# Performance work log

Measured on AMD Instinct MI355X. Metric: run time of the kernel, lower is better.

Reference implementation:

```python
import jax, jax.numpy as jnp
import numpy as np

H, B, T = 4, 16, 4000
E, D, A, C, K, O = 512, 512, 128, 10, 101, 512


def setup_inputs() -> dict:
    key = jax.random.key(0)
    ks = jax.random.split(key, 12)
    return {
        "enc_pad": jax.random.normal(ks[0], (B, T, E), jnp.float32),
        "enc_len": jax.random.randint(ks[1], (B,), T // 2, T + 1, jnp.int32),
        "dec_z": jax.random.normal(ks[2], (B, D), jnp.float32),
        "att_prev": jax.random.uniform(ks[3], (H, B, T), jnp.float32) / T,
        # learned parameters (per-head stacks)
        "Wenc": jax.random.normal(ks[4], (H, E, A), jnp.float32) / np.sqrt(E).astype(np.float32),
        "benc": jnp.zeros((H, A), jnp.float32),
        "Wdec": jax.random.normal(ks[5], (H, D, A), jnp.float32) / np.sqrt(D).astype(np.float32),
        "Watt": jax.random.normal(ks[6], (H, C, A), jnp.float32) / np.sqrt(C).astype(np.float32),
        "conv_w": jax.random.normal(ks[7], (H, C, K), jnp.float32) / np.sqrt(K).astype(np.float32),
        "gv": jax.random.normal(ks[8], (H, A), jnp.float32) / np.sqrt(A).astype(np.float32),
        "Wo": jax.random.normal(ks[9], (H * E, O), jnp.float32) / np.sqrt(H * E).astype(np.float32),
        "bo": jnp.zeros((O,), jnp.float32),
    }


def reference(enc_pad, enc_len, dec_z, att_prev, Wenc, benc, Wdec, Watt, conv_w, gv, Wo, bo):
    scaling = 1.0
    Hh, Bb, Tt = att_prev.shape
    Cc, Kk = conv_w.shape[1], conv_w.shape[2]
    pad_l = Kk // 2
    pad_r = Kk // 2 if Kk % 2 == 1 else Kk // 2 - 1
    # location conv: grouped 1D conv over heads. lhs [B,H,Tp], rhs [H*C,1,K]
    x = jnp.pad(att_prev.transpose(1, 0, 2), ((0, 0), (0, 0), (pad_l, pad_r)))
    rhs = conv_w.reshape(Hh * Cc, 1, Kk)
    conv = jax.lax.conv_general_dilated(
        x, rhs, window_strides=(1,), padding='VALID',
        dimension_numbers=('NCH', 'OIH', 'NCH'), feature_group_count=Hh)  # [B,H*C,T]
    conv = conv.reshape(Bb, Hh, Cc, Tt)
    att_conv = jnp.einsum('bhct,hca->bhta', conv, Watt)                    # mlp_att
    enc_proj = jnp.einsum('bte,hea->bhta', enc_pad, Wenc) + benc[None, :, None, :]  # mlp_enc
    dec_proj = jnp.einsum('bd,hda->bha', dec_z, Wdec)[:, :, None, :]       # mlp_dec
    e = jnp.einsum('bhta,ha->bht', jnp.tanh(enc_proj + dec_proj + att_conv), gv)  # gvec
    w = jax.nn.softmax(scaling * e, axis=-1)                               # [B,H,T]
    c = jnp.einsum('bht,bte->bhe', w, enc_pad).reshape(Bb, Hh * enc_pad.shape[-1])
    out = c @ Wo + bo                                                      # mlp_o
    return out, w.transpose(1, 0, 2)  # ws stacked as [H,B,T]
```

## Files before the change

kernel.cpp:

```cpp
#include <hip/hip_runtime.h>
#include <hip/hip_bf16.h>

#define H_ 4
#define B_ 16
#define T_ 4000
#define E_ 512
#define D_ 512
#define A_ 128
#define C_ 10
#define K_ 101
#define O_ 512
#define TC_ 50
#define CH_ (T_ / TC_)

typedef __attribute__((ext_vector_type(4))) float f32x4;
typedef __attribute__((ext_vector_type(8)))  short short8;

#define MFMA16(a, b, c) __builtin_amdgcn_mfma_f32_16x16x32_bf16(a, b, c, 0, 0, 0)

#define GLL16(gp, lp) __builtin_amdgcn_global_load_lds( \
    (const __attribute__((address_space(1))) unsigned int*)(gp), \
    (__attribute__((address_space(3))) unsigned int*)(lp), 16, 0, 0)

static __device__ __forceinline__ unsigned short f2bf(float x) {
  unsigned u = __float_as_uint(x);
  unsigned r = (u + 0x7FFFu + ((u >> 16) & 1u)) >> 16;
  return (unsigned short)r;
}
static __device__ __forceinline__ unsigned pk2(float a, float b) {
  return (unsigned)f2bf(a) | ((unsigned)f2bf(b) << 16);
}
static __device__ __forceinline__ unsigned cvtpk(float lo, float hi) {
  unsigned r;
  asm("v_cvt_pk_bf16_f32 %0, %1, %2" : "=v"(r) : "v"(lo), "v"(hi));
  return r;
}
static __device__ __forceinline__ uint4 packbf8(float4 f0, float4 f1) {
  uint4 u;
  u.x = cvtpk(f0.x, f0.y); u.y = cvtpk(f0.z, f0.w);
  u.z = cvtpk(f1.x, f1.y); u.w = cvtpk(f1.z, f1.w);
  return u;
}
static __device__ __forceinline__ float tanh_fast(float x) {
  return 1.0f - 2.0f / (__expf(2.0f * x) + 1.0f);
}
static __device__ __forceinline__ float bfup(unsigned short u) {
  return __uint_as_float((unsigned)u << 16);
}
static __device__ __forceinline__ int swz(int r) {
  return (r & 3) ^ ((r >> 2) & 3);
}

__global__ __launch_bounds__(256) void k_prepconv(
    const float* __restrict__ Wenc, const float* __restrict__ Watt,
    const float* __restrict__ dec_z, const float* __restrict__ Wdec,
    const float* __restrict__ benc, const float* __restrict__ att_prev,
    const float* __restrict__ conv_w,
    char* __restrict__ wbs2, char* __restrict__ wattb2,
    float* __restrict__ addv4, char* __restrict__ convpad) {
  __shared__ float ap[256 + K_ - 1 + 3];
  __shared__ float cw[C_ * K_];
  const int bid = blockIdx.x;
  const int tid = threadIdx.x;
  if (bid >= 257) {
    const int cid = bid - 257;
    const int bh = cid & 63;
    const int b = bh / H_, h = bh % H_;
    const int t0 = (cid >> 6) * 256;
    const float* src = att_prev + ((size_t)h * B_ + b) * T_;
    for (int i = tid; i < 256 + K_ - 1; i += 256) {
      int tt = t0 - (K_ / 2) + i;
      ap[i] = (tt >= 0 && tt < T_) ? src[tt] : 0.f;
    }
    for (int i = tid; i < C_ * K_; i += 256) cw[i] = conv_w[(size_t)h * C_ * K_ + i];
    __syncthreads();
    const int t = t0 + tid;
    if (t < T_) {
      float s[C_];
#pragma unroll
      for (int c = 0; c < C_; ++c) s[c] = 0.f;
      for (int k = 0; k < K_; ++k) {
        float apv = ap[tid + k];
#pragma unroll
        for (int c = 0; c < C_; ++c) s[c] += cw[c * K_ + k] * apv;
      }
      uint4 u0, u1;
      u0.x = pk2(s[0], s[1]); u0.y = pk2(s[2], s[3]);
      u0.z = pk2(s[4], s[5]); u0.w = pk2(s[6], s[7]);
      u1.x = pk2(s[8], s[9]); u1.y = 0u; u1.z = 0u; u1.w = 0u;
      char* dst = convpad + (size_t)(b * T_ + t) * 128 + h * 32;
      *(uint4*)dst = u0;
      *(uint4*)(dst + 16) = u1;
    }
  } else if (bid < 128) {
    const int c = bid * 256 + tid;
    const int kt = c >> 11;
    const int ci = c & 2047;
    const int col = ci >> 2, cc = ci & 3;
    const int h = col >> 7, a = col & 127;
    const int kk = kt * 32 + ((cc ^ swz(col)) & 3) * 8;
    const float* w = Wenc + ((size_t)h * E_ + kk) * A_ + a;
    uint4 u;
    u.x = pk2(w[0], w[A_]);
    u.y = pk2(w[2 * A_], w[3 * A_]);
    u.z = pk2(w[4 * A_], w[5 * A_]);
    u.w = pk2(w[6 * A_], w[7 * A_]);
    ((uint4*)wbs2)[c] = u;
  } else if (bid == 128) {
#pragma unroll
    for (int q = 0; q < 4; ++q) {
      const int cw2 = q * 256 + tid;
      const int h = cw2 >> 8;
      const int rr = cw2 & 255;
      const int col = rr >> 1, half = rr & 1;
      unsigned short v[8];
#pragma unroll
      for (int j = 0; j < 8; ++j) {
        const int k = half * 8 + j;
        v[j] = (k < C_) ? f2bf(Watt[((size_t)h * C_ + k) * A_ + col]) : (unsigned short)0;
      }
      uint4 u;
      u.x = (unsigned)v[0] | ((unsigned)v[1] << 16);
      u.y = (unsigned)v[2] | ((unsigned)v[3] << 16);
      u.z = (unsigned)v[4] | ((unsigned)v[5] << 16);
      u.w = (unsigned)v[6] | ((unsigned)v[7] << 16);
      ((uint4*)wattb2)[cw2] = u;
    }
  } else {
    const int idx = bid - 129;
    const int b = idx >> 3, h = (idx >> 1) & 3, ks = idx & 1;
    const int a = tid & 127, kh = tid >> 7;
    const int p = ks * 2 + kh;
    const int d0 = p * 128;
    const float* z = dec_z + (size_t)b * D_ + d0;
    const float* w = Wdec + ((size_t)h * D_ + d0) * A_ + a;
    float s = (p == 0) ? benc[h * A_ + a] : 0.f;
#pragma unroll 8
    for (int d = 0; d < 128; ++d) s += z[d] * w[(size_t)d * A_];
    addv4[(((size_t)p * B_ + b) * H_ + h) * A_ + a] = s;
  }
}

__global__ __launch_bounds__(512, 4) void k_fused_e_mfma(
    const float* __restrict__ enc,
    const char*  __restrict__ wbs2,
    const char*  __restrict__ convpad,
    const char*  __restrict__ wattb2,
    const float* __restrict__ addv4,
    const float* __restrict__ gv,
    char* __restrict__ encbf,
    float* __restrict__ e_out) {
  __shared__ char smem[73728];
  const int tid = threadIdx.x;
  const int wv = tid >> 6;
  const int lane = tid & 63, l15 = lane & 15, lg = lane >> 4;
  const int m0 = blockIdx.x * 64;
  const int h = wv >> 1;
  const bool aRole = (wv < 4);

  f32x4 acc[4][4];
#pragma unroll
  for (int i = 0; i < 4; ++i)
#pragma unroll
    for (int j = 0; j < 4; ++j) acc[i][j] = (f32x4){0.f, 0.f, 0.f, 0.f};

  int aOff[4], bOff[4];
#pragma unroll
  for (int q = 0; q < 4; ++q) {
    const int row = q * 16 + l15;
    aOff[q] = row * 64 + (((lg ^ swz(row)) & 3) << 4);
    const int col = wv * 64 + q * 16 + l15;
    bOff[q] = col * 64 + (((lg ^ swz(col)) & 3) << 4);
  }

  const int arow = tid >> 2, ac = tid & 3;
  const int ks = ((ac ^ swz(arow)) & 3) * 8;
  const float* eR = enc + (size_t)(m0 + arow) * E_ + ks;
  const int wOff = arow * 64 + ac * 16;
  char* ebW = encbf + (size_t)(m0 + arow) * 1024 + ks * 2;
  const char* bsrc = wbs2 + (size_t)(wv - 4) * 8192 + lane * 16;
  char* bdstBase = smem + 8192 + (wv - 4) * 8192;

  float4 X0, X1;
  const float* eP = eR + 64;
  const char* bsP = bsrc + 32768;

  if (aRole) {
    float4 c0 = *(const float4*)eR;
    float4 c1 = *(const float4*)(eR + 4);
    X0 = *(const float4*)(eR + 32);
    X1 = *(const float4*)(eR + 36);
    uint4 pkv = packbf8(c0, c1);
    *(uint4*)(smem + wOff) = pkv;
    *(uint4*)ebW = pkv;
    asm volatile("s_waitcnt lgkmcnt(0)" ::: "memory");
  } else {
#pragma unroll
    for (int i = 0; i < 8; ++i)
      GLL16(bsrc + i * 1024, bdstBase + i * 1024);
    asm volatile("s_waitcnt vmcnt(0) lgkmcnt(0)" ::: "memory");
  }
  __builtin_amdgcn_sched_barrier(0);
  __builtin_amdgcn_s_barrier();

#pragma unroll 1
  for (int kt = 0; kt < 16; ++kt) {
    const int cur = kt & 1;
    const char* bufA = smem + cur * 4096;
    const char* bufB = smem + 8192 + cur * 32768;

    if (!aRole && kt < 15) {
      char* d = smem + 8192 + (cur ^ 1) * 32768 + (wv - 4) * 8192;
#pragma unroll
      for (int i = 0; i < 8; ++i)
        GLL16(bsP + i * 1024, d + i * 1024);
    }
    __builtin_amdgcn_sched_barrier(0);

    short8 aF[4];
#pragma unroll
    for (int q = 0; q < 4; ++q) aF[q] = *(const short8*)(bufA + aOff[q]);
#pragma unroll
    for (int qn = 0; qn < 4; ++qn) {
      short8 bF = *(const short8*)(bufB + bOff[qn]);
#pragma unroll
      for (int qm = 0; qm < 4; ++qm)
        acc[qm][qn] = MFMA16(aF[qm], bF, acc[qm][qn]);
    }

    if (aRole) {
      if (kt < 15) {
        uint4 pkv = packbf8(X0, X1);
        *(uint4*)(smem + (cur ^ 1) * 4096 + wOff) = pkv;
        *(uint4*)(ebW + (kt + 1) * 64) = pkv;
      }
      if (kt < 14) {
        X0 = *(const float4*)eP;
        X1 = *(const float4*)(eP + 4);
        eP += 32;
      }
    } else {
      bsP += 32768;
    }

    if (kt < 14) {
      if (aRole)
        asm volatile("s_waitcnt lgkmcnt(0)" ::: "memory");
      else
        asm volatile("s_waitcnt vmcnt(0) lgkmcnt(0)" ::: "memory");
    } else {
      asm volatile("s_waitcnt vmcnt(0) lgkmcnt(0)" ::: "memory");
    }
    __builtin_amdgcn_sched_barrier(0);
    __builtin_amdgcn_s_barrier();
  }

  {
    short8 zf;
#pragma unroll
    for (int i = 0; i < 8; ++i) zf[i] = 0;
    short8 cf[4], wf[4];
#pragma unroll
    for (int q = 0; q < 4; ++q) { cf[q] = zf; wf[q] = zf; }
    if (lg < 2) {
#pragma unroll
      for (int q = 0; q < 4; ++q) {
        const int row = m0 + q * 16 + l15;
        cf[q] = *(const short8*)(convpad + (size_t)row * 128 + h * 32 + lg * 16);
        const int col = (wv & 1) * 64 + q * 16 + l15;
        wf[q] = *(const short8*)(wattb2 + ((size_t)h * 128 + col) * 32 + lg * 16);
      }
    }
#pragma unroll
    for (int qm = 0; qm < 4; ++qm)
#pragma unroll
      for (int qn = 0; qn < 4; ++qn)
        acc[qm][qn] = MFMA16(cf[qm], wf[qn], acc[qm][qn]);
  }

  {
    const unsigned b0w = (unsigned)m0 / 4000u;
    const unsigned b1w = (unsigned)(m0 + 63) / 4000u;
    float av0[4], av1[4], gvr[4];
#pragma unroll
    for (int qn = 0; qn < 4; ++qn) {
      const int col = (wv & 1) * 64 + qn * 16 + l15;
      const int i0 = (int)b0w * 512 + h * 128 + col;
      const int i1 = (int)b1w * 512 + h * 128 + col;
      av0[qn] = addv4[i0] + addv4[8192 + i0] + addv4[16384 + i0] + addv4[24576 + i0];
      av1[qn] = addv4[i1] + addv4[8192 + i1] + addv4[16384 + i1] + addv4[24576 + i1];
      gvr[qn] = gv[h * 128 + col];
    }
    float* Pb = (float*)smem;
#pragma unroll
    for (int qm = 0; qm < 4; ++qm) {
#pragma unroll
      for (int r = 0; r < 4; ++r) {
        const int rowLocal = qm * 16 + lg * 4 + r;
        const unsigned brow = (unsigned)(m0 + rowLocal);
        const unsigned bb = brow / 4000u;
        const int sel = (bb != b0w);
        float s = 0.f;
#pragma unroll
        for (int qn = 0; qn < 4; ++qn)
          s += gvr[qn] * tanh_fast(acc[qm][qn][r] + (sel ? av1[qn] : av0[qn]));
        s += __shfl_xor(s, 1);
        s += __shfl_xor(s, 2);
        s += __shfl_xor(s, 4);
        s += __shfl_xor(s, 8);
        if (l15 == 0) Pb[wv * 64 + rowLocal] = s;
      }
    }
  }
  __syncthreads();
  if (tid < 256) {
    const float* Pb = (const float*)smem;
    const int hh = tid >> 6, r = tid & 63;
    const float ev = Pb[(hh * 2) * 64 + r] + Pb[(hh * 2 + 1) * 64 + r];
    const unsigned brow = (unsigned)(m0 + r);
    const unsigned bb = brow / 4000u;
    const unsigned tt = brow - bb * 4000u;
    e_out[((size_t)bb * H_ + hh) * T_ + tt] = ev;
  }
}

__global__ __launch_bounds__(256) void k_msum(const float* __restrict__ e_in,
                                              float2* __restrict__ msum) {
  const int bh = blockIdx.x;
  const float* er = e_in + (size_t)bh * T_;
  __shared__ float red[256];
  const int tid = threadIdx.x;
  float m = -1e30f;
  for (int t = tid; t < T_; t += 256) m = fmaxf(m, er[t]);
  red[tid] = m;
  __syncthreads();
  for (int s = 128; s > 0; s >>= 1) {
    if (tid < s) red[tid] = fmaxf(red[tid], red[tid + s]);
    __syncthreads();
  }
  m = red[0];
  __syncthreads();
  float sum = 0.f;
  for (int t = tid; t < T_; t += 256) sum += __expf(er[t] - m);
  red[tid] = sum;
  __syncthreads();
  for (int s = 128; s > 0; s >>= 1) {
    if (tid < s) red[tid] += red[tid + s];
    __syncthreads();
  }
  if (tid == 0) msum[bh] = make_float2(m, 1.0f / red[0]);
}

__global__ __launch_bounds__(512) void k_ctx(const char* __restrict__ encbf,
                                             const float* __restrict__ e_in,
                                             const float2* __restrict__ msum,
                                             float* __restrict__ wout,
                                             float* __restrict__ partial) {
  const int b = blockIdx.x, tc = blockIdx.y;
  const int t0 = tc * CH_;
  const int tid = threadIdx.x;
  const int grp = tid >> 7, lt = tid & 127;
  __shared__ float wls[H_ * CH_];
  __shared__ float4 red[3][4][128];
  for (int i = tid; i < H_ * CH_; i += 512) {
    const int h = i / CH_, tt = i - h * CH_;
    const float2 ms = msum[b * H_ + h];
    const float w = __expf(e_in[((size_t)b * H_ + h) * T_ + t0 + tt] - ms.x) * ms.y;
    wls[i] = w;
    wout[((size_t)h * B_ + b) * T_ + t0 + tt] = w;
  }
  __syncthreads();
  float4 a0 = {0,0,0,0}, a1 = {0,0,0,0}, a2 = {0,0,0,0}, a3 = {0,0,0,0};
  const unsigned short* eb = (const unsigned short*)encbf;
  const int tg = grp * 20;
  const size_t ebase = ((size_t)b * T_ + t0 + tg) * 512 + lt * 4;
#pragma unroll 5
  for (int tt = 0; tt < 20; ++tt) {
    const ushort4 v = *(const ushort4*)(eb + ebase + (size_t)tt * 512);
    const float4 x = {bfup(v.x), bfup(v.y), bfup(v.z), bfup(v.w)};
    const float w0 = wls[tg + tt];
    const float w1 = wls[CH_ + tg + tt];
    const float w2 = wls[2 * CH_ + tg + tt];
    const float w3 = wls[3 * CH_ + tg + tt];
    a0.x += w0 * x.x; a0.y += w0 * x.y; a0.z += w0 * x.z; a0.w += w0 * x.w;
    a1.x += w1 * x.x; a1.y += w1 * x.y; a1.z += w1 * x.z; a1.w += w1 * x.w;
    a2.x += w2 * x.x; a2.y += w2 * x.y; a2.z += w2 * x.z; a2.w += w2 * x.w;
    a3.x += w3 * x.x; a3.y += w3 * x.y; a3.z += w3 * x.z; a3.w += w3 * x.w;
  }
  if (grp > 0) {
    red[grp - 1][0][lt] = a0;
    red[grp - 1][1][lt] = a1;
    red[grp - 1][2][lt] = a2;
    red[grp - 1][3][lt] = a3;
  }
  __syncthreads();
  if (grp == 0) {
#pragma unroll
    for (int g = 0; g < 3; ++g) {
      const float4 r0 = red[g][0][lt], r1 = red[g][1][lt];
      const float4 r2 = red[g][2][lt], r3 = red[g][3][lt];
      a0.x += r0.x; a0.y += r0.y; a0.z += r0.z; a0.w += r0.w;
      a1.x += r1.x; a1.y += r1.y; a1.z += r1.z; a1.w += r1.w;
      a2.x += r2.x; a2.y += r2.y; a2.z += r2.z; a2.w += r2.w;
      a3.x += r3.x; a3.y += r3.y; a3.z += r3.z; a3.w += r3.w;
    }
    float4* p4 = (float4*)partial;
    const size_t pbase = (((size_t)tc * B_ + b) * H_) * 128 + lt;
    p4[pbase] = a0;
    p4[pbase + 128] = a1;
    p4[pbase + 256] = a2;
    p4[pbase + 384] = a3;
  }
}

__global__ __launch_bounds__(256) void k_out_part(const float* __restrict__ partial,
                                                  const float* __restrict__ Wo,
                                                  float* __restrict__ p2) {
  const int b = blockIdx.x;
  const int o = blockIdx.y * 256 + threadIdx.x;
  const int kc = blockIdx.z;
  __shared__ float cS[256];
  const int he0 = kc * 256;
  {
    float s = 0.f;
#pragma unroll
    for (int tc = 0; tc < TC_; ++tc)
      s += partial[((size_t)tc * B_ + b) * (H_ * E_) + he0 + threadIdx.x];
    cS[threadIdx.x] = s;
  }
  __syncthreads();
  float s = 0.f;
#pragma unroll 8
  for (int i = 0; i < 256; ++i) s += cS[i] * Wo[(size_t)(he0 + i) * O_ + o];
  p2[((size_t)kc * B_ + b) * O_ + o] = s;
}

__global__ __launch_bounds__(512) void k_out_fin(const float* __restrict__ p2,
                                                 const float* __restrict__ bo,
                                                 float* __restrict__ out) {
  const int b = blockIdx.x, o = threadIdx.x;
  float s = bo[o];
#pragma unroll
  for (int kc = 0; kc < 8; ++kc) s += p2[((size_t)kc * B_ + b) * O_ + o];
  out[b * O_ + o] = s;
}

extern "C" void kernel_launch(void* const* d_in, const int* in_sizes, int n_in,
                              void* d_out, int out_size, void* d_ws, size_t ws_size,
                              hipStream_t stream) {
  (void)in_sizes; (void)n_in; (void)out_size; (void)ws_size;
  const float* enc      = (const float*)d_in[0];
  const float* dec_z    = (const float*)d_in[2];
  const float* att_prev = (const float*)d_in[3];
  const float* Wenc     = (const float*)d_in[4];
  const float* benc     = (const float*)d_in[5];
  const float* Wdec     = (const float*)d_in[6];
  const float* Watt     = (const float*)d_in[7];
  const float* conv_w   = (const float*)d_in[8];
  const float* gv       = (const float*)d_in[9];
  const float* Wo       = (const float*)d_in[10];
  const float* bo       = (const float*)d_in[11];

  float* out  = (float*)d_out;
  float* wout = out + B_ * O_;

  char* wsb = (char*)d_ws;
  float*  e_buf   = (float*)(wsb);
  char*   convpad = wsb + 1024000;
  char*   wbs2    = wsb + 9216000;
  char*   wattb2  = wsb + 9740288;
  float*  addv4   = (float*)(wsb + 9756672);
  float2* msum    = (float2*)(wsb + 9887744);
  float*  partial = (float*)(wsb + 9888256);
  float*  p2      = (float*)(wsb + 16441856);
  char*   encbf   = wsb + 16704000;

  hipLaunchKernelGGL(k_prepconv, dim3(1281), dim3(256), 0, stream,
                     Wenc, Watt, dec_z, Wdec, benc, att_prev, conv_w,
                     wbs2, wattb2, addv4, convpad);
  hipLaunchKernelGGL(k_fused_e_mfma, dim3(1000), dim3(512), 0, stream,
                     enc, wbs2, convpad, wattb2, addv4, gv, encbf, e_buf);
  hipLaunchKernelGGL(k_msum, dim3(B_ * H_), dim3(256), 0, stream, e_buf, msum);
  hipLaunchKernelGGL(k_ctx, dim3(B_, TC_), dim3(512), 0, stream,
                     encbf, e_buf, msum, wout, partial);
  hipLaunchKernelGGL(k_out_part, dim3(B_, O_ / 256, 8), dim3(256), 0, stream, partial, Wo, p2);
  hipLaunchKernelGGL(k_out_fin, dim3(B_), dim3(512), 0, stream, p2, bo, out);
}
```

Measured before the change: 129.3 us.

## Replace softmax max pass with static bound from sum of absolute gv

Replaces the per-row max reduction with a per-head constant bound sum|gv|, valid because tanh lies in [-1,1]. The softmax sum kernel then needs only one pass, is split into four chunks per row across 256 blocks, and accumulates with atomics into sums zeroed in the prep kernel. This removes one full read of e and the serial tree reductions. It adds underflow risk if e sits far below the bound, and a division replaces the reciprocal multiply in the context kernel.

```diff
diff --git a/kernel.cpp b/kernel.cpp
--- a/kernel.cpp
+++ b/kernel.cpp
@@ -55,9 +55,10 @@
     const float* __restrict__ Wenc, const float* __restrict__ Watt,
     const float* __restrict__ dec_z, const float* __restrict__ Wdec,
     const float* __restrict__ benc, const float* __restrict__ att_prev,
-    const float* __restrict__ conv_w,
+    const float* __restrict__ conv_w, const float* __restrict__ gv,
     char* __restrict__ wbs2, char* __restrict__ wattb2,
-    float* __restrict__ addv4, char* __restrict__ convpad) {
+    float* __restrict__ addv4, char* __restrict__ convpad,
+    float* __restrict__ msM, float* __restrict__ sums) {
   __shared__ float ap[256 + K_ - 1 + 3];
   __shared__ float cw[C_ * K_];
   const int bid = blockIdx.x;
@@ -126,6 +127,13 @@
       u.w = (unsigned)v[6] | ((unsigned)v[7] << 16);
       ((uint4*)wattb2)[cw2] = u;
     }
+    if (tid < 4) {
+      float m = 0.f;
+#pragma unroll 8
+      for (int a = 0; a < A_; ++a) m += fabsf(gv[tid * A_ + a]);
+      msM[tid] = m;
+    }
+    if (tid >= 4 && tid < 68) sums[tid - 4] = 0.f;
   } else {
     const int idx = bid - 129;
     const int b = idx >> 3, h = (idx >> 1) & 3, ks = idx & 1;
@@ -324,36 +332,32 @@
   }
 }
 
-__global__ __launch_bounds__(256) void k_msum(const float* __restrict__ e_in,
-                                              float2* __restrict__ msum) {
-  const int bh = blockIdx.x;
-  const float* er = e_in + (size_t)bh * T_;
-  __shared__ float red[256];
-  const int tid = threadIdx.x;
-  float m = -1e30f;
-  for (int t = tid; t < T_; t += 256) m = fmaxf(m, er[t]);
-  red[tid] = m;
+__global__ __launch_bounds__(256) void k_sums(const float* __restrict__ e_in,
+                                              const float* __restrict__ msM,
+                                              float* __restrict__ sums) {
+  const int bh = blockIdx.x >> 2;
+  const int chunk = blockIdx.x & 3;
+  const float M = msM[bh & 3];
+  const float* er = e_in + (size_t)bh * T_ + chunk * 1000;
+  float s = 0.f;
+  for (int t = threadIdx.x; t < 1000; t += 256) s += __expf(er[t] - M);
+  s += __shfl_xor(s, 1);
+  s += __shfl_xor(s, 2);
+  s += __shfl_xor(s, 4);
+  s += __shfl_xor(s, 8);
+  s += __shfl_xor(s, 16);
+  s += __shfl_xor(s, 32);
+  __shared__ float ws[4];
+  if ((threadIdx.x & 63) == 0) ws[threadIdx.x >> 6] = s;
   __syncthreads();
-  for (int s = 128; s > 0; s >>= 1) {
-    if (tid < s) red[tid] = fmaxf(red[tid], red[tid + s]);
-    __syncthreads();
-  }
-  m = red[0];
-  __syncthreads();
-  float sum = 0.f;
-  for (int t = tid; t < T_; t += 256) sum += __expf(er[t] - m);
-  red[tid] = sum;
-  __syncthreads();
-  for (int s = 128; s > 0; s >>= 1) {
-    if (tid < s) red[tid] += red[tid + s];
-    __syncthreads();
-  }
-  if (tid == 0) msum[bh] = make_float2(m, 1.0f / red[0]);
+  if (threadIdx.x == 0)
+    atomicAdd(&sums[bh], ws[0] + ws[1] + ws[2] + ws[3]);
 }
 
 __global__ __launch_bounds__(512) void k_ctx(const char* __restrict__ encbf,
                                              const float* __restrict__ e_in,
-                                             const float2* __restrict__ msum,
+                                             const float* __restrict__ msM,
+                                             const float* __restrict__ sums,
                                              float* __restrict__ wout,
                                              float* __restrict__ partial) {
   const int b = blockIdx.x, tc = blockIdx.y;
@@ -364,8 +368,8 @@
   __shared__ float4 red[3][4][128];
   for (int i = tid; i < H_ * CH_; i += 512) {
     const int h = i / CH_, tt = i - h * CH_;
-    const float2 ms = msum[b * H_ + h];
-    const float w = __expf(e_in[((size_t)b * H_ + h) * T_ + t0 + tt] - ms.x) * ms.y;
+    const float w = __expf(e_in[((size_t)b * H_ + h) * T_ + t0 + tt] - msM[h]) /
+                    sums[b * H_ + h];
     wls[i] = w;
     wout[((size_t)h * B_ + b) * T_ + t0 + tt] = w;
   }
@@ -470,19 +474,20 @@
   char*   wbs2    = wsb + 9216000;
   char*   wattb2  = wsb + 9740288;
   float*  addv4   = (float*)(wsb + 9756672);
-  float2* msum    = (float2*)(wsb + 9887744);
+  float*  msM     = (float*)(wsb + 9887744);
+  float*  sums    = (float*)(wsb + 9887808);
   float*  partial = (float*)(wsb + 9888256);
   float*  p2      = (float*)(wsb + 16441856);
   char*   encbf   = wsb + 16704000;
 
   hipLaunchKernelGGL(k_prepconv, dim3(1281), dim3(256), 0, stream,
-                     Wenc, Watt, dec_z, Wdec, benc, att_prev, conv_w,
-                     wbs2, wattb2, addv4, convpad);
+                     Wenc, Watt, dec_z, Wdec, benc, att_prev, conv_w, gv,
+                     wbs2, wattb2, addv4, convpad, msM, sums);
   hipLaunchKernelGGL(k_fused_e_mfma, dim3(1000), dim3(512), 0, stream,
                      enc, wbs2, convpad, wattb2, addv4, gv, encbf, e_buf);
-  hipLaunchKernelGGL(k_msum, dim3(B_ * H_), dim3(256), 0, stream, e_buf, msum);
+  hipLaunchKernelGGL(k_sums, dim3(256), dim3(256), 0, stream, e_buf, msM, sums);
   hipLaunchKernelGGL(k_ctx, dim3(B_, TC_), dim3(512), 0, stream,
-                     encbf, e_buf, msum, wout, partial);
+                     encbf, e_buf, msM, sums, wout, partial);
   hipLaunchKernelGGL(k_out_part, dim3(B_, O_ / 256, 8), dim3(256), 0, stream, partial, Wo, p2);
   hipLaunchKernelGGL(k_out_fin, dim3(B_), dim3(512), 0, stream, p2, bo, out);
 }
```

Result: no change. 128.7 us (-0.4%).
